# Performance work log

Hardware: AMD Instinct MI355X
Metric: run time of the kernel (lower is better)

The kernel has to match this reference:

```python
import jax, jax.numpy as jnp
import numpy as np
import math

B, H, S, D = 2, 16, 2048, 64

def setup_inputs() -> dict:
    key = jax.random.key(0)
    kq, kk, kv = jax.random.split(key, 3)
    Q = jax.random.normal(kq, (B, H, S, D), dtype=jnp.float32)
    K = jax.random.normal(kk, (B, H, S, D), dtype=jnp.float32)
    V = jax.random.normal(kv, (B, H, S, D), dtype=jnp.float32)
    attn_mask = jnp.ones((B, 1, S, S), dtype=jnp.int32)
    return {"Q": Q, "K": K, "V": V, "attn_mask": attn_mask}

def reference(Q, K, V, attn_mask):
    # scores: [B, H, S, S]
    scores = jnp.einsum('bhqd,bhkd->bhqk', Q, K) / math.sqrt(D)
    scores = jnp.where(attn_mask == 0, jnp.float32(-1e9), scores)
    attn_prob = jax.nn.softmax(scores, axis=-1)
    # dropout p=0.0 (eval): identity
    context = jnp.einsum('bhqk,bhkd->bhqd', attn_prob, V)
    return (context, attn_prob)
```

## Files before the change

kernel.cpp:

```cpp
#include <hip/hip_runtime.h>
#include <math.h>

constexpr int Bc = 2, Hc = 16, Sc = 2048, Dc = 64;
constexpr int BM = 64;
constexpr int BN = 64;
constexpr int LDQ = 72;
constexpr int LDV = 66;
constexpr float SCALE = 0.125f;

typedef __bf16 bf16_t;
typedef __bf16 bf16x8 __attribute__((ext_vector_type(8)));
typedef __bf16 bf16x4 __attribute__((ext_vector_type(4)));
typedef __bf16 bf16x2 __attribute__((ext_vector_type(2)));
typedef float floatx4 __attribute__((ext_vector_type(4)));

#define MFMA16(a, b, c) __builtin_amdgcn_mfma_f32_16x16x32_bf16((a), (b), (c), 0, 0, 0)

__global__ __launch_bounds__(256, 2)
void sdpa_fused_kernel(const float* __restrict__ Q, const float* __restrict__ K,
                       const float* __restrict__ V, const int* __restrict__ Mask,
                       float* __restrict__ CtxOut, float* __restrict__ ProbOut)
{
    __shared__ bf16_t Qs[BM * LDQ];
    __shared__ bf16_t Ks[BN * LDQ];
    __shared__ bf16_t Vs[BN * LDV];
    __shared__ bf16_t Ps[BM * LDQ];

    const int tid  = threadIdx.x;
    const int wave = tid >> 6;
    const int lane = tid & 63;
    const int quad = lane >> 4;
    const int l16  = lane & 15;

    const int qt    = blockIdx.x;
    const int bh    = blockIdx.y;
    const int b     = bh >> 4;
    const int qbase = qt * BM;

    const float* Qp = Q + ((size_t)bh * Sc + qbase) * Dc;
    const float* Kp = K + (size_t)bh * Sc * Dc;
    const float* Vp = V + (size_t)bh * Sc * Dc;
    const int*   Mp = Mask + (size_t)b * Sc * Sc;
    float* Pg = ProbOut + (size_t)bh * Sc * Sc;
    float* Cg = CtxOut + ((size_t)bh * Sc + qbase) * Dc;

    #pragma unroll
    for (int t = 0; t < 4; ++t) {
        int i = tid + t * 256;
        int r = i >> 4;
        int c = (i & 15) << 2;
        float4 v = *reinterpret_cast<const float4*>(Qp + r * Dc + c);
        bf16x4 w; w[0] = (bf16_t)v.x; w[1] = (bf16_t)v.y; w[2] = (bf16_t)v.z; w[3] = (bf16_t)v.w;
        *reinterpret_cast<bf16x4*>(&Qs[r * LDQ + c]) = w;
    }
    __syncthreads();

    const int qrow_lds = wave * 16 + l16;
    bf16x8 qa0 = *reinterpret_cast<const bf16x8*>(&Qs[qrow_lds * LDQ + quad * 8]);
    bf16x8 qa1 = *reinterpret_cast<const bf16x8*>(&Qs[qrow_lds * LDQ + 32 + quad * 8]);

    float m_i[4], l_i[4];
    #pragma unroll
    for (int r = 0; r < 4; ++r) { m_i[r] = -3.0e38f; l_i[r] = 0.f; }

    const int mrow0 = qbase + wave * 16 + quad * 4;

    for (int kt = 0; kt < Sc / BN; ++kt) {
        __syncthreads();
        const float* Kt = Kp + (size_t)kt * BN * Dc;
        #pragma unroll
        for (int t = 0; t < 4; ++t) {
            int i = tid + t * 256;
            int r = i >> 4;
            int c = (i & 15) << 2;
            float4 v = *reinterpret_cast<const float4*>(Kt + r * Dc + c);
            bf16x4 w; w[0] = (bf16_t)v.x; w[1] = (bf16_t)v.y; w[2] = (bf16_t)v.z; w[3] = (bf16_t)v.w;
            *reinterpret_cast<bf16x4*>(&Ks[r * LDQ + c]) = w;
        }
        __syncthreads();

        floatx4 acc[4];
        #pragma unroll
        for (int nt = 0; nt < 4; ++nt) acc[nt] = (floatx4){0.f, 0.f, 0.f, 0.f};
        #pragma unroll
        for (int nt = 0; nt < 4; ++nt) {
            const bf16_t* kr = &Ks[(nt * 16 + l16) * LDQ + quad * 8];
            bf16x8 kb0 = *reinterpret_cast<const bf16x8*>(kr);
            bf16x8 kb1 = *reinterpret_cast<const bf16x8*>(kr + 32);
            acc[nt] = MFMA16(qa0, kb0, acc[nt]);
            acc[nt] = MFMA16(qa1, kb1, acc[nt]);
        }
        const int kcol0 = kt * BN;
        #pragma unroll
        for (int nt = 0; nt < 4; ++nt) {
            #pragma unroll
            for (int r = 0; r < 4; ++r) {
                float sv = acc[nt][r] * SCALE;
                int mv = Mp[(size_t)(mrow0 + r) * Sc + kcol0 + nt * 16 + l16];
                acc[nt][r] = mv ? sv : -1e9f;
            }
        }
        #pragma unroll
        for (int r = 0; r < 4; ++r) {
            float mx = fmaxf(fmaxf(acc[0][r], acc[1][r]), fmaxf(acc[2][r], acc[3][r]));
            #pragma unroll
            for (int off = 1; off < 16; off <<= 1) mx = fmaxf(mx, __shfl_xor(mx, off, 64));
            float mn = fmaxf(m_i[r], mx);
            float sum = __expf(acc[0][r] - mn) + __expf(acc[1][r] - mn) +
                        __expf(acc[2][r] - mn) + __expf(acc[3][r] - mn);
            #pragma unroll
            for (int off = 1; off < 16; off <<= 1) sum += __shfl_xor(sum, off, 64);
            l_i[r] = l_i[r] * __expf(m_i[r] - mn) + sum;
            m_i[r] = mn;
        }
    }

    float linv[4];
    #pragma unroll
    for (int r = 0; r < 4; ++r) linv[r] = 1.0f / l_i[r];

    floatx4 co[4];
    #pragma unroll
    for (int dt = 0; dt < 4; ++dt) co[dt] = (floatx4){0.f, 0.f, 0.f, 0.f};

    for (int kt = 0; kt < Sc / BN; ++kt) {
        __syncthreads();
        const float* Kt = Kp + (size_t)kt * BN * Dc;
        const float* Vt = Vp + (size_t)kt * BN * Dc;
        #pragma unroll
        for (int t = 0; t < 4; ++t) {
            int i = tid + t * 256;
            int r = i >> 4;
            int c = (i & 15) << 2;
            float4 v = *reinterpret_cast<const float4*>(Kt + r * Dc + c);
            bf16x4 w; w[0] = (bf16_t)v.x; w[1] = (bf16_t)v.y; w[2] = (bf16_t)v.z; w[3] = (bf16_t)v.w;
            *reinterpret_cast<bf16x4*>(&Ks[r * LDQ + c]) = w;
            float4 u = *reinterpret_cast<const float4*>(Vt + r * Dc + c);
            bf16x2 x0; x0[0] = (bf16_t)u.x; x0[1] = (bf16_t)u.y;
            bf16x2 x1; x1[0] = (bf16_t)u.z; x1[1] = (bf16_t)u.w;
            *reinterpret_cast<bf16x2*>(&Vs[r * LDV + c]) = x0;
            *reinterpret_cast<bf16x2*>(&Vs[r * LDV + c + 2]) = x1;
        }
        __syncthreads();

        floatx4 acc[4];
        #pragma unroll
        for (int nt = 0; nt < 4; ++nt) acc[nt] = (floatx4){0.f, 0.f, 0.f, 0.f};
        #pragma unroll
        for (int nt = 0; nt < 4; ++nt) {
            const bf16_t* kr = &Ks[(nt * 16 + l16) * LDQ + quad * 8];
            bf16x8 kb0 = *reinterpret_cast<const bf16x8*>(kr);
            bf16x8 kb1 = *reinterpret_cast<const bf16x8*>(kr + 32);
            acc[nt] = MFMA16(qa0, kb0, acc[nt]);
            acc[nt] = MFMA16(qa1, kb1, acc[nt]);
        }
        const int kcol0 = kt * BN;
        #pragma unroll
        for (int nt = 0; nt < 4; ++nt) {
            #pragma unroll
            for (int r = 0; r < 4; ++r) {
                float sv = acc[nt][r] * SCALE;
                int mv = Mp[(size_t)(mrow0 + r) * Sc + kcol0 + nt * 16 + l16];
                sv = mv ? sv : -1e9f;
                float p = __expf(sv - m_i[r]) * linv[r];
                Pg[(size_t)(mrow0 + r) * Sc + kcol0 + nt * 16 + l16] = p;
                Ps[(wave * 16 + quad * 4 + r) * LDQ + nt * 16 + l16] = (bf16_t)p;
            }
        }
        __syncthreads();

        #pragma unroll
        for (int ks = 0; ks < 2; ++ks) {
            bf16x8 pa = *reinterpret_cast<const bf16x8*>(
                &Ps[(wave * 16 + l16) * LDQ + ks * 32 + quad * 8]);
            #pragma unroll
            for (int dt = 0; dt < 4; ++dt) {
                bf16x8 vb;
                #pragma unroll
                for (int j = 0; j < 8; ++j)
                    vb[j] = Vs[(ks * 32 + quad * 8 + j) * LDV + dt * 16 + l16];
                co[dt] = MFMA16(pa, vb, co[dt]);
            }
        }
    }

    #pragma unroll
    for (int dt = 0; dt < 4; ++dt) {
        #pragma unroll
        for (int r = 0; r < 4; ++r) {
            Cg[(size_t)(wave * 16 + quad * 4 + r) * Dc + dt * 16 + l16] = co[dt][r];
        }
    }
}

extern "C" void kernel_launch(void* const* d_in, const int* in_sizes, int n_in,
                              void* d_out, int out_size, void* d_ws, size_t ws_size,
                              hipStream_t stream) {
    const float* Q    = (const float*)d_in[0];
    const float* K    = (const float*)d_in[1];
    const float* V    = (const float*)d_in[2];
    const int*   mask = (const int*)d_in[3];

    float* ctx  = (float*)d_out;
    float* prob = (float*)d_out + (size_t)Bc * Hc * Sc * Dc;

    dim3 grid(Sc / BM, Bc * Hc);
    sdpa_fused_kernel<<<grid, 256, 0, stream>>>(Q, K, V, mask, ctx, prob);
}
```

Baseline: 1.019 ms.

## Prefetch K/V tiles in registers, transpose V in LDS, hoist mask loads

Global loads of the next K (and V) tile are issued into registers before the current tile is computed, so load latency overlaps with MFMA and softmax work. V is stored transposed in LDS with a 16-byte aligned stride, which turns the eight scalar LDS reads per MFMA operand into one vector read. Mask loads are gathered before the QK MFMAs, and the barrier between the Ps write and the PV MFMA is removed because each wave reads only its own Ps rows. In exchange the kernel uses more registers, which may lower occupancy, and the transposed V stores are scalar 2-byte LDS writes.

```diff
diff --git a/kernel.cpp b/kernel.cpp
--- a/kernel.cpp
+++ b/kernel.cpp
@@ -5,13 +5,13 @@
 constexpr int BM = 64;
 constexpr int BN = 64;
 constexpr int LDQ = 72;
-constexpr int LDV = 66;
+constexpr int LDV = 72;
+constexpr int NKT = Sc / BN;
 constexpr float SCALE = 0.125f;
 
 typedef __bf16 bf16_t;
 typedef __bf16 bf16x8 __attribute__((ext_vector_type(8)));
 typedef __bf16 bf16x4 __attribute__((ext_vector_type(4)));
-typedef __bf16 bf16x2 __attribute__((ext_vector_type(2)));
 typedef float floatx4 __attribute__((ext_vector_type(4)));
 
 #define MFMA16(a, b, c) __builtin_amdgcn_mfma_f32_16x16x32_bf16((a), (b), (c), 0, 0, 0)
@@ -21,10 +21,10 @@
                        const float* __restrict__ V, const int* __restrict__ Mask,
                        float* __restrict__ CtxOut, float* __restrict__ ProbOut)
 {
-    __shared__ bf16_t Qs[BM * LDQ];
-    __shared__ bf16_t Ks[BN * LDQ];
-    __shared__ bf16_t Vs[BN * LDV];
-    __shared__ bf16_t Ps[BM * LDQ];
+    __shared__ __align__(16) bf16_t Qs[BM * LDQ];
+    __shared__ __align__(16) bf16_t Ks[BN * LDQ];
+    __shared__ __align__(16) bf16_t Vt[Dc * LDV];
+    __shared__ __align__(16) bf16_t Ps[BM * LDQ];
 
     const int tid  = threadIdx.x;
     const int wave = tid >> 6;
@@ -64,20 +64,47 @@
     for (int r = 0; r < 4; ++r) { m_i[r] = -3.0e38f; l_i[r] = 0.f; }
 
     const int mrow0 = qbase + wave * 16 + quad * 4;
-
-    for (int kt = 0; kt < Sc / BN; ++kt) {
-        __syncthreads();
-        const float* Kt = Kp + (size_t)kt * BN * Dc;
+    const int* mr[4]; float* pr[4];
+    #pragma unroll
+    for (int r = 0; r < 4; ++r) {
+        mr[r] = Mp + (size_t)(mrow0 + r) * Sc;
+        pr[r] = Pg + (size_t)(mrow0 + r) * Sc;
+    }
+
+    float4 kreg[4];
+    #pragma unroll
+    for (int t = 0; t < 4; ++t) {
+        int i = tid + t * 256;
+        kreg[t] = *reinterpret_cast<const float4*>(Kp + (i >> 4) * Dc + ((i & 15) << 2));
+    }
+    for (int kt = 0; kt < NKT; ++kt) {
+        __syncthreads();
         #pragma unroll
         for (int t = 0; t < 4; ++t) {
             int i = tid + t * 256;
             int r = i >> 4;
             int c = (i & 15) << 2;
-            float4 v = *reinterpret_cast<const float4*>(Kt + r * Dc + c);
-            bf16x4 w; w[0] = (bf16_t)v.x; w[1] = (bf16_t)v.y; w[2] = (bf16_t)v.z; w[3] = (bf16_t)v.w;
+            bf16x4 w; w[0] = (bf16_t)kreg[t].x; w[1] = (bf16_t)kreg[t].y;
+                      w[2] = (bf16_t)kreg[t].z; w[3] = (bf16_t)kreg[t].w;
             *reinterpret_cast<bf16x4*>(&Ks[r * LDQ + c]) = w;
         }
-        __syncthreads();
+        if (kt + 1 < NKT) {
+            const float* Kn = Kp + (size_t)(kt + 1) * BN * Dc;
+            #pragma unroll
+            for (int t = 0; t < 4; ++t) {
+                int i = tid + t * 256;
+                kreg[t] = *reinterpret_cast<const float4*>(Kn + (i >> 4) * Dc + ((i & 15) << 2));
+            }
+        }
+        __syncthreads();
+
+        const int kc = kt * BN + l16;
+        int mv[4][4];
+        #pragma unroll
+        for (int nt = 0; nt < 4; ++nt)
+            #pragma unroll
+            for (int r = 0; r < 4; ++r)
+                mv[nt][r] = mr[r][kc + nt * 16];
 
         floatx4 acc[4];
         #pragma unroll
@@ -90,14 +117,12 @@
             acc[nt] = MFMA16(qa0, kb0, acc[nt]);
             acc[nt] = MFMA16(qa1, kb1, acc[nt]);
         }
-        const int kcol0 = kt * BN;
         #pragma unroll
         for (int nt = 0; nt < 4; ++nt) {
             #pragma unroll
             for (int r = 0; r < 4; ++r) {
                 float sv = acc[nt][r] * SCALE;
-                int mv = Mp[(size_t)(mrow0 + r) * Sc + kcol0 + nt * 16 + l16];
-                acc[nt][r] = mv ? sv : -1e9f;
+                acc[nt][r] = mv[nt][r] ? sv : -1e9f;
             }
         }
         #pragma unroll
@@ -123,25 +148,48 @@
     #pragma unroll
     for (int dt = 0; dt < 4; ++dt) co[dt] = (floatx4){0.f, 0.f, 0.f, 0.f};
 
-    for (int kt = 0; kt < Sc / BN; ++kt) {
-        __syncthreads();
-        const float* Kt = Kp + (size_t)kt * BN * Dc;
-        const float* Vt = Vp + (size_t)kt * BN * Dc;
+    float4 vreg[4];
+    #pragma unroll
+    for (int t = 0; t < 4; ++t) {
+        int i = tid + t * 256;
+        kreg[t] = *reinterpret_cast<const float4*>(Kp + (i >> 4) * Dc + ((i & 15) << 2));
+        vreg[t] = *reinterpret_cast<const float4*>(Vp + (size_t)lane * Dc + 4 * (4 * wave + t));
+    }
+    for (int kt = 0; kt < NKT; ++kt) {
+        __syncthreads();
         #pragma unroll
         for (int t = 0; t < 4; ++t) {
             int i = tid + t * 256;
             int r = i >> 4;
             int c = (i & 15) << 2;
-            float4 v = *reinterpret_cast<const float4*>(Kt + r * Dc + c);
-            bf16x4 w; w[0] = (bf16_t)v.x; w[1] = (bf16_t)v.y; w[2] = (bf16_t)v.z; w[3] = (bf16_t)v.w;
+            bf16x4 w; w[0] = (bf16_t)kreg[t].x; w[1] = (bf16_t)kreg[t].y;
+                      w[2] = (bf16_t)kreg[t].z; w[3] = (bf16_t)kreg[t].w;
             *reinterpret_cast<bf16x4*>(&Ks[r * LDQ + c]) = w;
-            float4 u = *reinterpret_cast<const float4*>(Vt + r * Dc + c);
-            bf16x2 x0; x0[0] = (bf16_t)u.x; x0[1] = (bf16_t)u.y;
-            bf16x2 x1; x1[0] = (bf16_t)u.z; x1[1] = (bf16_t)u.w;
-            *reinterpret_cast<bf16x2*>(&Vs[r * LDV + c]) = x0;
-            *reinterpret_cast<bf16x2*>(&Vs[r * LDV + c + 2]) = x1;
-        }
-        __syncthreads();
+            const int d0 = 4 * (4 * wave + t);
+            Vt[(d0 + 0) * LDV + lane] = (bf16_t)vreg[t].x;
+            Vt[(d0 + 1) * LDV + lane] = (bf16_t)vreg[t].y;
+            Vt[(d0 + 2) * LDV + lane] = (bf16_t)vreg[t].z;
+            Vt[(d0 + 3) * LDV + lane] = (bf16_t)vreg[t].w;
+        }
+        if (kt + 1 < NKT) {
+            const float* Kn = Kp + (size_t)(kt + 1) * BN * Dc;
+            const float* Vn = Vp + (size_t)(kt + 1) * BN * Dc;
+            #pragma unroll
+            for (int t = 0; t < 4; ++t) {
+                int i = tid + t * 256;
+                kreg[t] = *reinterpret_cast<const float4*>(Kn + (i >> 4) * Dc + ((i & 15) << 2));
+                vreg[t] = *reinterpret_cast<const float4*>(Vn + (size_t)lane * Dc + 4 * (4 * wave + t));
+            }
+        }
+        __syncthreads();
+
+        const int kc = kt * BN + l16;
+        int mv[4][4];
+        #pragma unroll
+        for (int nt = 0; nt < 4; ++nt)
+            #pragma unroll
+            for (int r = 0; r < 4; ++r)
+                mv[nt][r] = mr[r][kc + nt * 16];
 
         floatx4 acc[4];
         #pragma unroll
@@ -154,31 +202,25 @@
             acc[nt] = MFMA16(qa0, kb0, acc[nt]);
             acc[nt] = MFMA16(qa1, kb1, acc[nt]);
         }
-        const int kcol0 = kt * BN;
         #pragma unroll
         for (int nt = 0; nt < 4; ++nt) {
             #pragma unroll
             for (int r = 0; r < 4; ++r) {
                 float sv = acc[nt][r] * SCALE;
-                int mv = Mp[(size_t)(mrow0 + r) * Sc + kcol0 + nt * 16 + l16];
-                sv = mv ? sv : -1e9f;
+                sv = mv[nt][r] ? sv : -1e9f;
                 float p = __expf(sv - m_i[r]) * linv[r];
-                Pg[(size_t)(mrow0 + r) * Sc + kcol0 + nt * 16 + l16] = p;
+                pr[r][kc + nt * 16] = p;
                 Ps[(wave * 16 + quad * 4 + r) * LDQ + nt * 16 + l16] = (bf16_t)p;
             }
         }
-        __syncthreads();
-
         #pragma unroll
         for (int ks = 0; ks < 2; ++ks) {
             bf16x8 pa = *reinterpret_cast<const bf16x8*>(
                 &Ps[(wave * 16 + l16) * LDQ + ks * 32 + quad * 8]);
             #pragma unroll
             for (int dt = 0; dt < 4; ++dt) {
-                bf16x8 vb;
-                #pragma unroll
-                for (int j = 0; j < 8; ++j)
-                    vb[j] = Vs[(ks * 32 + quad * 8 + j) * LDV + dt * 16 + l16];
+                bf16x8 vb = *reinterpret_cast<const bf16x8*>(
+                    &Vt[(dt * 16 + l16) * LDV + ks * 32 + quad * 8]);
                 co[dt] = MFMA16(pa, vb, co[dt]);
             }
         }
```

Measured after the change: 855.3 us. 16.0% less time.
